# Kernel tuning notes

Hardware: AMD Instinct MI355X
Metric: run time of the kernel (lower is better)

The kernel has to match this reference:

```python
import jax, jax.numpy as jnp
import numpy as np

N_TREES = 512
DEPTH = 10
NODES_PER_TREE = 2 ** DEPTH - 1  # 1023, heap-indexed complete binary tree
N = N_TREES * NODES_PER_TREE     # 523776 nodes
X_SIZE = 128
H_SIZE = 128
NUM_CLASSES = 5
VOCAB = 32000


def _level_ids(l):
    """Global node ids for level l (root=0) and their child ids (None for leaves)."""
    start = 2 ** l - 1
    heap = start + np.arange(2 ** l)
    tree_off = np.arange(N_TREES)[:, None] * NODES_PER_TREE
    ids = (tree_off + heap[None, :]).reshape(-1)
    if l < DEPTH - 1:
        child_heap = np.stack([2 * heap + 1, 2 * heap + 2], axis=-1)  # [2^l, 2]
        child = (np.arange(N_TREES)[:, None, None] * NODES_PER_TREE
                 + child_heap[None]).reshape(-1, 2)
        return jnp.asarray(ids), jnp.asarray(child)
    return jnp.asarray(ids), None


def setup_inputs() -> dict:
    key = jax.random.key(0)
    ks = jax.random.split(key, 12)
    s = 0.05
    return {
        "wordid": jax.random.randint(ks[0], (N,), 0, VOCAB),
        "E":      jax.random.normal(ks[1], (VOCAB, X_SIZE), jnp.float32) * s,
        "W_iou":  jax.random.normal(ks[2], (3 * H_SIZE, X_SIZE), jnp.float32) * s,
        "b_iou":  jax.random.normal(ks[3], (3 * H_SIZE,), jnp.float32) * s,
        "U_iou":  jax.random.normal(ks[4], (3 * H_SIZE, H_SIZE), jnp.float32) * s,
        "b_Uiou": jax.random.normal(ks[5], (3 * H_SIZE,), jnp.float32) * s,
        "W_f":    jax.random.normal(ks[6], (H_SIZE, X_SIZE), jnp.float32) * s,
        "b_Wf":   jax.random.normal(ks[7], (H_SIZE,), jnp.float32) * s,
        "U_f":    jax.random.normal(ks[8], (H_SIZE, H_SIZE), jnp.float32) * s,
        "b_Uf":   jax.random.normal(ks[9], (H_SIZE,), jnp.float32) * s,
        "W_out":  jax.random.normal(ks[10], (NUM_CLASSES, H_SIZE), jnp.float32) * s,
        "b_out":  jax.random.normal(ks[11], (NUM_CLASSES,), jnp.float32) * s,
    }


def reference(wordid, E, W_iou, b_iou, U_iou, b_Uiou, W_f, b_Wf, U_f, b_Uf, W_out, b_out):
    mask = (wordid != -1)  # PAD_WORD mask; all-true for generated ids
    x = E[wordid * mask.astype(wordid.dtype)] * mask[:, None].astype(E.dtype)  # [N, X]

    h = jnp.zeros((N, H_SIZE), E.dtype)
    c = jnp.zeros((N, H_SIZE), E.dtype)

    # Topological traversal: leaves (deepest level) up to roots.
    for l in reversed(range(DEPTH)):
        ids, child = _level_ids(l)
        xl = x[ids]  # [M, X]
        if child is None:  # leaves: empty mailbox -> h_tild = c_tild = 0
            h_tild = jnp.zeros((ids.shape[0], H_SIZE), E.dtype)
            c_tild = h_tild
        else:
            hc = h[child]                               # mailbox h: [M, 2, H]
            cc = c[child]                               # mailbox c: [M, 2, H]
            h_tild = hc.sum(axis=1)                     # child-sum
            wx = xl @ W_f.T + b_Wf                      # [M, H]
            uh = hc @ U_f.T + b_Uf                      # [M, 2, H]
            f = jax.nn.sigmoid(wx[:, None, :] + uh)     # per-child forget gate
            c_tild = (f * cc).sum(axis=1)
        iou = xl @ W_iou.T + b_iou + h_tild @ U_iou.T + b_Uiou  # [M, 3H]
        i, o, u = jnp.split(iou, 3, axis=1)
        i, o, u = jax.nn.sigmoid(i), jax.nn.sigmoid(o), jnp.tanh(u)
        cl = i * u + c_tild
        hl = o * jnp.tanh(cl)
        h = h.at[ids].set(hl)
        c = c.at[ids].set(cl)

    # dropout is identity in eval / p=0.0
    logits = h @ W_out.T + b_out  # [N, num_classes]
    return logits
```

## Files before the change

### kernel.cpp

```cpp
#include <hip/hip_runtime.h>
#include <hip/hip_bf16.h>

#define H 128
#define TDEPTH 10
#define NPT 1023
#define NTREES 512

typedef unsigned short bf16_t;
typedef unsigned int u32;
typedef __attribute__((ext_vector_type(8))) short bf16x8;
typedef __attribute__((ext_vector_type(4))) float f32x4;

__device__ __forceinline__ float rcp_(float x) { return __builtin_amdgcn_rcpf(x); }
__device__ __forceinline__ float sig_(float x) { return rcp_(1.0f + __expf(-x)); }
__device__ __forceinline__ float th_(float x)  { return 1.0f - 2.0f * rcp_(__expf(2.0f * x) + 1.0f); }
__device__ __forceinline__ float b2f(u32 u) {
    union { float f; u32 u; } v; v.u = u << 16; return v.f;
}
__device__ __forceinline__ bf16_t f2b16(float f) {
    __hip_bfloat16 h = __float2bfloat16(f);
    return *reinterpret_cast<bf16_t*>(&h);
}
__device__ __forceinline__ bf16x8 ld8(const bf16_t* p) {
    return *reinterpret_cast<const bf16x8*>(p);
}
__device__ __forceinline__ bf16x8 ld8c(const char* p) {
    return *reinterpret_cast<const bf16x8*>(p);
}
__device__ __forceinline__ void gload16(const void* g, void* l) {
    __builtin_amdgcn_global_load_lds(
        (const __attribute__((address_space(1))) void*)g,
        (__attribute__((address_space(3))) void*)l, 16, 0, 0);
}
#define MFMA(a,b,c) __builtin_amdgcn_mfma_f32_16x16x32_bf16(a,b,c,0,0,0)

#define R_H  8192
#define R_C  24576
#define BUFSZ 40960

#define FX_SZ   24576
#define F_H     49152
#define F_C     65536
#define F_LDSSZ 81920

__global__ void pack_weights(const float* __restrict__ W_iou, const float* __restrict__ U_iou,
                             const float* __restrict__ W_f,   const float* __restrict__ U_f,
                             const float* __restrict__ W_out, bf16_t* __restrict__ Wb)
{
    int i = blockIdx.x * 256 + threadIdx.x;
    if (i < 131072) {
        int k    = i & 127;
        int p    = (i >> 7) & 7;
        int feat = i >> 10;
        float v;
        switch (p) {
            case 0: v = W_iou[(      feat) * H + k]; break;
            case 1: v = W_iou[(128 + feat) * H + k]; break;
            case 2: v = W_iou[(256 + feat) * H + k]; break;
            case 3: v = U_iou[(      feat) * H + k]; break;
            case 4: v = U_iou[(128 + feat) * H + k]; break;
            case 5: v = U_iou[(256 + feat) * H + k]; break;
            case 6: v = W_f  [feat * H + k]; break;
            default: v = U_f [feat * H + k]; break;
        }
        Wb[i] = f2b16(v);
    } else {
        int j = i - 131072;
        int cls = j >> 7, k = j & 127;
        Wb[i] = f2b16(cls < 5 ? W_out[cls * H + k] : 0.0f);
    }
}

__global__ void pack_E(const float* __restrict__ E, bf16_t* __restrict__ Eb)
{
    int i = blockIdx.x * 256 + threadIdx.x;
    Eb[i] = f2b16(E[i]);
}

__global__ __launch_bounds__(512, 2) void leaf8_fused(
    const int* __restrict__ wordid, const bf16_t* __restrict__ Eb,
    const bf16_t* __restrict__ Wb,
    const float* __restrict__ b_iou, const float* __restrict__ b_Uiou,
    const float* __restrict__ b_Wf,  const float* __restrict__ b_Uf,
    bf16_t* __restrict__ h_cur, bf16_t* __restrict__ c_cur,
    const float* __restrict__ b_out, float* __restrict__ out,
    int t0, int nt)
{
    extern __shared__ __align__(16) char lds_raw[];

    const int tid  = threadIdx.x;
    const int lane = tid & 63;
    const int w    = tid >> 6;
    const int l15  = lane & 15;
    const int kg   = lane >> 4;
    const int feat = w * 16 + l15;
    const int tilebase = blockIdx.x * nt;

    const float bi  = b_iou[      feat] + b_Uiou[      feat];
    const float bo  = b_iou[128 + feat] + b_Uiou[128 + feat];
    const float bu  = b_iou[256 + feat] + b_Uiou[256 + feat];
    const float bfv = b_Wf[feat] + b_Uf[feat];
    const f32x4 z = {0.f, 0.f, 0.f, 0.f};

    const bf16_t* wbase = Wb + (size_t)feat * 1024 + kg * 8;
    const bf16_t* Wob   = Wb + 131072;

    const int lrow = lane >> 4;
    const int colb = (lane & 15) * 16;

    struct Wids { int a, b, c; };
    auto loadwid = [&](int t) -> Wids {
        Wids r;
        int tb64 = (tilebase + t) * 64, tb32 = (tilebase + t) * 32;
        {   int gl = tb64 + w * 4 + lrow;
            int tt = gl >> 9, ii = gl & 511;
            r.a = wordid[(t0 + tt) * NPT + 511 + ii]; }
        {   int gl = tb64 + 32 + w * 4 + lrow;
            int tt = gl >> 9, ii = gl & 511;
            r.b = wordid[(t0 + tt) * NPT + 511 + ii]; }
        {   int gp = tb32 + w * 4 + lrow;
            int tt = gp >> 8, ii = gp & 255;
            r.c = wordid[(t0 + tt) * NPT + 255 + ii]; }
        return r;
    };

    auto issue = [&](const Wids& wd, char* xbuf) {
        {   int row = w * 4 + lrow;
            gload16((const char*)Eb + (size_t)wd.a * 256 + (colb ^ ((row & 7) << 4)),
                    xbuf + w * 1024); }
        {   int row = 32 + w * 4 + lrow;
            gload16((const char*)Eb + (size_t)wd.b * 256 + (colb ^ ((row & 7) << 4)),
                    xbuf + (w + 8) * 1024); }
        {   int row = w * 4 + lrow;
            gload16((const char*)Eb + (size_t)wd.c * 256 + (colb ^ ((row & 7) << 4)),
                    xbuf + (w + 16) * 1024); }
    };

    Wids wcur = loadwid(0);
    issue(wcur, lds_raw);
    if (nt > 1) wcur = loadwid(1);
    __syncthreads();

    char* h_s = lds_raw + F_H;
    char* c_s = lds_raw + F_C;

    for (int t = 0; t < nt; ++t) {
        char* xbuf  = lds_raw + (t & 1) * FX_SZ;
        char* xleaf = xbuf;
        char* xpar  = xbuf + 16384;
        const int n0 = (tilebase + t) * 32;

        f32x4 lac[3][4];
#pragma unroll
        for (int g = 0; g < 3; ++g)
#pragma unroll
            for (int m = 0; m < 4; ++m) lac[g][m] = z;

#pragma unroll
        for (int ks = 0; ks < 4; ++ks) {
            bf16x8 W0 = ld8(wbase + ks * 32 + 0 * 128);
            bf16x8 W1 = ld8(wbase + ks * 32 + 1 * 128);
            bf16x8 W2 = ld8(wbase + ks * 32 + 2 * 128);
            const int cb = (ks * 32 + kg * 8) * 2;
#pragma unroll
            for (int mt = 0; mt < 4; ++mt) {
                int row = mt * 16 + l15;
                bf16x8 xa = ld8c(xleaf + row * 256 + (cb ^ ((row & 7) << 4)));
                lac[0][mt] = MFMA(xa, W0, lac[0][mt]);
                lac[1][mt] = MFMA(xa, W1, lac[1][mt]);
                lac[2][mt] = MFMA(xa, W2, lac[2][mt]);
            }
        }

        if (t + 1 < nt) {
            issue(wcur, lds_raw + ((t + 1) & 1) * FX_SZ);
            if (t + 2 < nt) wcur = loadwid(t + 2);
        }

#pragma unroll
        for (int mt = 0; mt < 4; ++mt) {
#pragma unroll
            for (int r = 0; r < 4; ++r) {
                int j = mt * 16 + kg * 4 + r;
                float iv = sig_(lac[0][mt][r] + bi);
                float ov = sig_(lac[1][mt][r] + bo);
                float uv = th_ (lac[2][mt][r] + bu);
                float cl = iv * uv;
                float hl = ov * th_(cl);
                int off = j * 256 + ((feat * 2) ^ (((j >> 1) & 7) << 4));
                *(bf16_t*)(h_s + off) = f2b16(hl);
                *(bf16_t*)(c_s + off) = f2b16(cl);
            }
        }
        __syncthreads();

        f32x4 acc[6][2];
#pragma unroll
        for (int g = 0; g < 6; ++g)
#pragma unroll
            for (int m = 0; m < 2; ++m) acc[g][m] = z;

#pragma unroll
        for (int ks = 0; ks < 4; ++ks) {
            bf16x8 W0 = ld8(wbase + ks * 32 + 0 * 128);
            bf16x8 W1 = ld8(wbase + ks * 32 + 1 * 128);
            bf16x8 W2 = ld8(wbase + ks * 32 + 2 * 128);
            bf16x8 W3 = ld8(wbase + ks * 32 + 3 * 128);
            bf16x8 W4 = ld8(wbase + ks * 32 + 4 * 128);
            bf16x8 W5 = ld8(wbase + ks * 32 + 5 * 128);
            bf16x8 W6 = ld8(wbase + ks * 32 + 6 * 128);
            bf16x8 W7 = ld8(wbase + ks * 32 + 7 * 128);
            const int cb = (ks * 32 + kg * 8) * 2;
#pragma unroll
            for (int mt = 0; mt < 2; ++mt) {
                const int row = mt * 16 + l15;
                const int sw  = (row & 7) << 4;
                bf16x8 xa  = ld8c(xpar + row * 256 + (cb ^ sw));
                bf16x8 h0a = ld8c(h_s + (2 * row)     * 256 + (cb ^ sw));
                bf16x8 h1a = ld8c(h_s + (2 * row + 1) * 256 + (cb ^ sw));
                acc[0][mt] = MFMA(h1a, W3, MFMA(h0a, W3, MFMA(xa, W0, acc[0][mt])));
                acc[1][mt] = MFMA(h1a, W4, MFMA(h0a, W4, MFMA(xa, W1, acc[1][mt])));
                acc[2][mt] = MFMA(h1a, W5, MFMA(h0a, W5, MFMA(xa, W2, acc[2][mt])));
                acc[3][mt] = MFMA(xa,  W6, acc[3][mt]);
                acc[4][mt] = MFMA(h0a, W7, acc[4][mt]);
                acc[5][mt] = MFMA(h1a, W7, acc[5][mt]);
            }
        }

        if (w < 4) {
            const int pr = (w & 2) ? 1 : 0;
            const int mbase = (w & 1) * 16;
            f32x4 lacc = z;
#pragma unroll
            for (int ks = 0; ks < 4; ++ks) {
                const int cb = (ks * 32 + kg * 8) * 2;
                int prow = mbase + l15;
                bf16x8 ha = ld8c(h_s + (size_t)(2 * prow + pr) * 256
                                 + (cb ^ ((prow & 7) << 4)));
                bf16x8 wo = ld8(Wob + (size_t)l15 * 128 + ks * 32 + kg * 8);
                lacc = MFMA(ha, wo, lacc);
            }
            if (l15 < 5) {
                float bo5 = b_out[l15];
#pragma unroll
                for (int r = 0; r < 4; ++r) {
                    int m  = mbase + kg * 4 + r;
                    int gc = 2 * (n0 + m) + pr;
                    int tt = gc >> 9, ii = gc & 511;
                    out[(size_t)((t0 + tt) * NPT + 511 + ii) * 5 + l15] = lacc[r] + bo5;
                }
            }
        }

#pragma unroll
        for (int mt = 0; mt < 2; ++mt) {
#pragma unroll
            for (int r = 0; r < 4; ++r) {
                int nb = mt * 16 + kg * 4 + r;
                int g  = n0 + nb;
                float iv = sig_(acc[0][mt][r] + bi);
                float ov = sig_(acc[1][mt][r] + bo);
                float uv = th_ (acc[2][mt][r] + bu);
                float fx = acc[3][mt][r];
                float f0 = sig_(fx + acc[4][mt][r] + bfv);
                float f1 = sig_(fx + acc[5][mt][r] + bfv);
                int co = (feat * 2) ^ ((nb & 7) << 4);
                float c0 = b2f((u32)*(const bf16_t*)(c_s + (2 * nb)     * 256 + co));
                float c1 = b2f((u32)*(const bf16_t*)(c_s + (2 * nb + 1) * 256 + co));
                float cl = iv * uv + f0 * c0 + f1 * c1;
                float hl = ov * th_(cl);
                h_cur[(size_t)g * H + feat] = f2b16(hl);
                c_cur[(size_t)g * H + feat] = f2b16(cl);
            }
        }

        __syncthreads();
    }
}

__global__ __launch_bounds__(512, 2) void internal_mfma(
    const int* __restrict__ wordid, const bf16_t* __restrict__ Eb,
    const bf16_t* __restrict__ Wb,
    const float* __restrict__ b_iou, const float* __restrict__ b_Uiou,
    const float* __restrict__ b_Wf,  const float* __restrict__ b_Uf,
    const bf16_t* __restrict__ h_prev, const bf16_t* __restrict__ c_prev,
    bf16_t* __restrict__ h_cur, bf16_t* __restrict__ c_cur,
    const float* __restrict__ b_out, float* __restrict__ out,
    int level, int t0, int nt)
{
    extern __shared__ __align__(16) char lds_raw[];

    const int tid  = threadIdx.x;
    const int lane = tid & 63;
    const int w    = tid >> 6;
    const int l15  = lane & 15;
    const int kg   = lane >> 4;
    const int feat = w * 16 + l15;
    const int tilebase = blockIdx.x * nt;

    const float bi  = b_iou[      feat] + b_Uiou[      feat];
    const float bo  = b_iou[128 + feat] + b_Uiou[128 + feat];
    const float bu  = b_iou[256 + feat] + b_Uiou[256 + feat];
    const float bfv = b_Wf[feat] + b_Uf[feat];
    const f32x4 z = {0.f, 0.f, 0.f, 0.f};

    const bf16_t* wbase = Wb + (size_t)feat * 1024 + kg * 8;
    const bf16_t* Wob   = Wb + 131072;

    const int lrow = lane >> 4;
    const int colb = (lane & 15) * 16;

    auto issue = [&](int t, char* buf) {
        int n0 = (tilebase + t) * 32;
#pragma unroll
        for (int cc = 0; cc < 5; ++cc) {
            int ch = w + cc * 8;
            const char* src;
            if (ch < 8) {
                int row = ch * 4 + lrow;
                int g = n0 + row;
                int tt = g >> level, ii = g & ((1 << level) - 1);
                int wid = wordid[(t0 + tt) * NPT + (1 << level) - 1 + ii];
                src = (const char*)Eb + (size_t)wid * 256 + (colb ^ ((row & 7) << 4));
            } else if (ch < 24) {
                int row = (ch - 8) * 4 + lrow;
                src = (const char*)h_prev + ((size_t)(2 * n0) + row) * 256
                    + (colb ^ (((row >> 1) & 7) << 4));
            } else {
                int row = (ch - 24) * 4 + lrow;
                src = (const char*)c_prev + ((size_t)(2 * n0) + row) * 256
                    + (colb ^ (((row >> 1) & 7) << 4));
            }
            gload16(src, buf + ch * 1024);
        }
    };

    issue(0, lds_raw);
    __syncthreads();

    for (int t = 0; t < nt; ++t) {
        char* buf = lds_raw + (t & 1) * BUFSZ;
        char* x_s = buf;
        char* h_s = buf + R_H;
        char* c_s = buf + R_C;
        const int n0 = (tilebase + t) * 32;

        f32x4 acc[6][2];
#pragma unroll
        for (int g = 0; g < 6; ++g)
#pragma unroll
            for (int m = 0; m < 2; ++m) acc[g][m] = z;

#pragma unroll
        for (int ks = 0; ks < 4; ++ks) {
            const int cb = (ks * 32 + kg * 8) * 2;
            bf16x8 W0 = ld8(wbase + ks * 32 + 0 * 128);
            bf16x8 W1 = ld8(wbase + ks * 32 + 1 * 128);
            bf16x8 W2 = ld8(wbase + ks * 32 + 2 * 128);
            bf16x8 W3 = ld8(wbase + ks * 32 + 3 * 128);
            bf16x8 W4 = ld8(wbase + ks * 32 + 4 * 128);
            bf16x8 W5 = ld8(wbase + ks * 32 + 5 * 128);
            bf16x8 W6 = ld8(wbase + ks * 32 + 6 * 128);
            bf16x8 W7 = ld8(wbase + ks * 32 + 7 * 128);
#pragma unroll
            for (int mt = 0; mt < 2; ++mt) {
                const int row = mt * 16 + l15;
                const int sw  = (row & 7) << 4;
                bf16x8 xa  = ld8c(x_s + row * 256 + (cb ^ sw));
                bf16x8 h0a = ld8c(h_s + (2 * row)     * 256 + (cb ^ sw));
                bf16x8 h1a = ld8c(h_s + (2 * row + 1) * 256 + (cb ^ sw));
                acc[0][mt] = MFMA(h1a, W3, MFMA(h0a, W3, MFMA(xa, W0, acc[0][mt])));
                acc[1][mt] = MFMA(h1a, W4, MFMA(h0a, W4, MFMA(xa, W1, acc[1][mt])));
                acc[2][mt] = MFMA(h1a, W5, MFMA(h0a, W5, MFMA(xa, W2, acc[2][mt])));
                acc[3][mt] = MFMA(xa,  W6, acc[3][mt]);
                acc[4][mt] = MFMA(h0a, W7, acc[4][mt]);
                acc[5][mt] = MFMA(h1a, W7, acc[5][mt]);
            }
        }

        if (t + 1 < nt) issue(t + 1, lds_raw + ((t + 1) & 1) * BUFSZ);

        if (w < 4) {
            const int pr = (w & 2) ? 1 : 0;
            const int mbase = (w & 1) * 16;
            f32x4 lacc = z;
#pragma unroll
            for (int ks = 0; ks < 4; ++ks) {
                const int cb = (ks * 32 + kg * 8) * 2;
                int prow = mbase + l15;
                bf16x8 ha = ld8c(h_s + (size_t)(2 * prow + pr) * 256
                                 + (cb ^ ((prow & 7) << 4)));
                bf16x8 wo = ld8(Wob + (size_t)l15 * 128 + ks * 32 + kg * 8);
                lacc = MFMA(ha, wo, lacc);
            }
            if (l15 < 5) {
                float bo5 = b_out[l15];
                int lc = level + 1;
#pragma unroll
                for (int r = 0; r < 4; ++r) {
                    int m  = mbase + kg * 4 + r;
                    int gc = 2 * (n0 + m) + pr;
                    int tt = gc >> lc, ii = gc & ((1 << lc) - 1);
                    out[(size_t)((t0 + tt) * NPT + (1 << lc) - 1 + ii) * 5 + l15] = lacc[r] + bo5;
                }
            }
        }

#pragma unroll
        for (int mt = 0; mt < 2; ++mt) {
#pragma unroll
            for (int r = 0; r < 4; ++r) {
                int nb = mt * 16 + kg * 4 + r;
                int g  = n0 + nb;
                float iv = sig_(acc[0][mt][r] + bi);
                float ov = sig_(acc[1][mt][r] + bo);
                float uv = th_ (acc[2][mt][r] + bu);
                float fx = acc[3][mt][r];
                float f0 = sig_(fx + acc[4][mt][r] + bfv);
                float f1 = sig_(fx + acc[5][mt][r] + bfv);
                int co = (feat * 2) ^ ((nb & 7) << 4);
                float c0 = b2f((u32)*(const bf16_t*)(c_s + (2 * nb)     * 256 + co));
                float c1 = b2f((u32)*(const bf16_t*)(c_s + (2 * nb + 1) * 256 + co));
                float cl = iv * uv + f0 * c0 + f1 * c1;
                float hl = ov * th_(cl);
                h_cur[(size_t)g * H + feat] = f2b16(hl);
                c_cur[(size_t)g * H + feat] = f2b16(cl);
            }
        }

        __syncthreads();
    }
}

__global__ void logits_root(
    const bf16_t* __restrict__ h0buf, const float* __restrict__ W_out,
    const float* __restrict__ b_out, float* __restrict__ out,
    int M, int t0)
{
    int wv     = (blockIdx.x * blockDim.x + threadIdx.x) >> 6;
    int lane   = threadIdx.x & 63;
    int nwaves = (gridDim.x * blockDim.x) >> 6;
    for (int g = wv; g < M; g += nwaves) {
        float h0 = b2f((u32)h0buf[(size_t)g * H + lane]);
        float h1 = b2f((u32)h0buf[(size_t)g * H + 64 + lane]);
#pragma unroll
        for (int c = 0; c < 5; ++c) {
            float p = h0 * W_out[c * H + lane] + h1 * W_out[c * H + 64 + lane];
#pragma unroll
            for (int off = 32; off >= 1; off >>= 1) p += __shfl_xor(p, off, 64);
            if (lane == 0) out[(size_t)(t0 + g) * NPT * 5 + c] = p + b_out[c];
        }
    }
}

extern "C" void kernel_launch(void* const* d_in, const int* in_sizes, int n_in,
                              void* d_out, int out_size, void* d_ws, size_t ws_size,
                              hipStream_t stream)
{
    (void)in_sizes; (void)n_in; (void)out_size;
    const int*   wordid = (const int*)  d_in[0];
    const float* E      = (const float*)d_in[1];
    const float* W_iou  = (const float*)d_in[2];
    const float* b_iou  = (const float*)d_in[3];
    const float* U_iou  = (const float*)d_in[4];
    const float* b_Uiou = (const float*)d_in[5];
    const float* W_f    = (const float*)d_in[6];
    const float* b_Wf   = (const float*)d_in[7];
    const float* U_f    = (const float*)d_in[8];
    const float* b_Uf   = (const float*)d_in[9];
    const float* W_out  = (const float*)d_in[10];
    const float* b_out  = (const float*)d_in[11];
    float* out = (float*)d_out;

    bf16_t* Wb = (bf16_t*)d_ws;
    bf16_t* Eb = Wb + 133120;
    bf16_t* dyn = Eb + (size_t)32000 * H;
    const size_t fixed_bytes = (133120 + (size_t)32000 * H) * 2;

    int C = 1;
    while (C < 16 && fixed_bytes + (size_t)(NTREES / C) * 262144u > ws_size) C <<= 1;
    const int T = NTREES / C;

    bf16_t* hA = dyn;
    bf16_t* cA = hA + (size_t)T * 256 * H;
    bf16_t* hB = cA + (size_t)T * 256 * H;
    bf16_t* cB = hB + (size_t)T * 256 * H;

    pack_weights<<<520, 256, 0, stream>>>(W_iou, U_iou, W_f, U_f, W_out, Wb);
    pack_E<<<16000, 256, 0, stream>>>(E, Eb);

    for (int chunk = 0; chunk < C; ++chunk) {
        int t0 = chunk * T;

        {
            int tiles  = (T << 8) / 32;
            int blocks = tiles < 512 ? tiles : 512;
            int nt     = tiles / blocks;
            leaf8_fused<<<blocks, 512, F_LDSSZ, stream>>>(
                wordid, Eb, Wb, b_iou, b_Uiou, b_Wf, b_Uf,
                hB, cB, b_out, out, t0, nt);
        }

        for (int l = TDEPTH - 3; l >= 0; --l) {
            int M = T << l;
            bf16_t* h_cur  = (l & 1) ? hA : hB;
            bf16_t* c_cur  = (l & 1) ? cA : cB;
            bf16_t* h_prev = (l & 1) ? hB : hA;
            bf16_t* c_prev = (l & 1) ? cB : cA;

            int tiles  = M / 32;
            int blocks = tiles < 512 ? tiles : 512;
            if (blocks < 1) blocks = 1;
            int nt     = tiles / blocks;
            internal_mfma<<<blocks, 512, 2 * BUFSZ, stream>>>(
                wordid, Eb, Wb, b_iou, b_Uiou, b_Wf, b_Uf,
                h_prev, c_prev, h_cur, c_cur, b_out, out, l, t0, nt);
        }
        int blocksR = (T / 4 < 4096) ? ((T + 3) / 4) : 4096;
        if (blocksR < 1) blocksR = 1;
        logits_root<<<blocksR, 256, 0, stream>>>(hB, W_out, b_out, out, T, t0);
    }
}
```

Measured before the change: 343.3 us.

## Single-buffer parent embeddings in fused leaf kernel, halve internal-level grid

The fused leaf kernel stops double-buffering the parent-level embedding tile. It now loads it into a single LDS region at the start of each tile iteration, which shrinks LDS use from 80KB to 72KB. The intent is to raise occupancy or free LDS. The parent embedding load now overlaps only with the leaf MFMA phase instead of a whole iteration, so its latency may be exposed. The internal-level kernel grid is also capped at 256 blocks instead of 512, so each block handles more tiles.

```diff
diff --git a/kernel.cpp b/kernel.cpp
--- a/kernel.cpp
+++ b/kernel.cpp
@@ -38,10 +38,10 @@
 #define R_C  24576
 #define BUFSZ 40960
 
-#define FX_SZ   24576
-#define F_H     49152
-#define F_C     65536
-#define F_LDSSZ 81920
+#define F_XP    32768
+#define F_H     40960
+#define F_C     57344
+#define F_LDSSZ 73728
 
 __global__ void pack_weights(const float* __restrict__ W_iou, const float* __restrict__ U_iou,
                              const float* __restrict__ W_f,   const float* __restrict__ U_f,
@@ -124,31 +124,34 @@
         return r;
     };
 
-    auto issue = [&](const Wids& wd, char* xbuf) {
+    auto issue_leaf = [&](const Wids& wd, char* xbuf) {
         {   int row = w * 4 + lrow;
             gload16((const char*)Eb + (size_t)wd.a * 256 + (colb ^ ((row & 7) << 4)),
                     xbuf + w * 1024); }
         {   int row = 32 + w * 4 + lrow;
             gload16((const char*)Eb + (size_t)wd.b * 256 + (colb ^ ((row & 7) << 4)),
                     xbuf + (w + 8) * 1024); }
-        {   int row = w * 4 + lrow;
-            gload16((const char*)Eb + (size_t)wd.c * 256 + (colb ^ ((row & 7) << 4)),
-                    xbuf + (w + 16) * 1024); }
     };
-
-    Wids wcur = loadwid(0);
-    issue(wcur, lds_raw);
-    if (nt > 1) wcur = loadwid(1);
+    auto issue_xpar = [&](int widc) {
+        int row = w * 4 + lrow;
+        gload16((const char*)Eb + (size_t)widc * 256 + (colb ^ ((row & 7) << 4)),
+                lds_raw + F_XP + w * 1024);
+    };
+
+    Wids w0 = loadwid(0);
+    issue_leaf(w0, lds_raw);
+    int pwc = w0.c;
+    Wids wcur = (nt > 1) ? loadwid(1) : w0;
     __syncthreads();
 
     char* h_s = lds_raw + F_H;
     char* c_s = lds_raw + F_C;
 
     for (int t = 0; t < nt; ++t) {
-        char* xbuf  = lds_raw + (t & 1) * FX_SZ;
-        char* xleaf = xbuf;
-        char* xpar  = xbuf + 16384;
+        char* xleaf = lds_raw + (t & 1) * 16384;
         const int n0 = (tilebase + t) * 32;
+
+        issue_xpar(pwc);
 
         f32x4 lac[3][4];
 #pragma unroll
@@ -172,8 +175,10 @@
             }
         }
 
+        int pwc_next = pwc;
         if (t + 1 < nt) {
-            issue(wcur, lds_raw + ((t + 1) & 1) * FX_SZ);
+            issue_leaf(wcur, lds_raw + ((t + 1) & 1) * 16384);
+            pwc_next = wcur.c;
             if (t + 2 < nt) wcur = loadwid(t + 2);
         }
 
@@ -194,6 +199,7 @@
         }
         __syncthreads();
 
+        char* xpar = lds_raw + F_XP;
         f32x4 acc[6][2];
 #pragma unroll
         for (int g = 0; g < 6; ++g)
@@ -274,6 +280,7 @@
             }
         }
 
+        pwc = pwc_next;
         __syncthreads();
     }
 }
@@ -509,7 +516,7 @@
             bf16_t* c_prev = (l & 1) ? cB : cA;
 
             int tiles  = M / 32;
-            int blocks = tiles < 512 ? tiles : 512;
+            int blocks = tiles < 256 ? tiles : 256;
             if (blocks < 1) blocks = 1;
             int nt     = tiles / blocks;
             internal_mfma<<<blocks, 512, 2 * BUFSZ, stream>>>(
```

Result: faster. 321.4 us (-6.4%).
